# Optimization experiments

Measured on AMD Instinct MI355X. Metric: run time of the kernel, lower is better.

Reference implementation:

```python
import jax, jax.numpy as jnp
import numpy as np
from jax import lax

N_WIRES = 4
N_OPS = 30
BN_EPS = 1e-5


def _rl_ops():
    # Deterministic stand-in for tq.RandomLayer(n_ops=30): cycle rx/ry/rz/cnot.
    kinds = ['rx', 'ry', 'rz', 'cnot']
    ops, p = [], 0
    for i in range(N_OPS):
        k = kinds[i % 4]
        if k == 'cnot':
            ops.append((k, i % N_WIRES, (i + 1) % N_WIRES))
        else:
            ops.append((k, i % N_WIRES, p))
            p += 1
    return ops, p

RL_OPS, N_RL_PARAMS = _rl_ops()  # 23 rotation params, 7 cnots


def _rx(t):
    c = jnp.cos(t / 2).astype(jnp.complex64)
    s = (-1j * jnp.sin(t / 2).astype(jnp.complex64))
    return jnp.stack([jnp.stack([c, s], -1), jnp.stack([s, c], -1)], -2)


def _ry(t):
    c = jnp.cos(t / 2).astype(jnp.complex64)
    s = jnp.sin(t / 2).astype(jnp.complex64)
    return jnp.stack([jnp.stack([c, -s], -1), jnp.stack([s, c], -1)], -2)


def _rz(t):
    e = jnp.exp((-1j * t / 2).astype(jnp.complex64))
    z = jnp.zeros_like(e)
    return jnp.stack([jnp.stack([e, z], -1), jnp.stack([z, jnp.conj(e)], -1)], -2)


def _apply_1q(state, U, w):
    # state: [B,2,2,2,2]; U: [2,2] (shared) or [B,2,2] (per-sample)
    s = jnp.moveaxis(state, w + 1, -1)
    if U.ndim == 2:
        s = jnp.einsum('ij,b...j->b...i', U, s)
    else:
        s = jnp.einsum('bij,b...j->b...i', U, s)
    return jnp.moveaxis(s, -1, w + 1)


def _apply_cnot(state, c, t):
    s = jnp.moveaxis(state, (c + 1, t + 1), (-2, -1))
    s = s.at[..., 1, :].set(s[..., 1, ::-1])  # flip target where control==1
    return jnp.moveaxis(s, (-2, -1), (c + 1, t + 1))


# PauliZ expectation table: z[k, w] = +/-1 for basis state k on wire w
_ZTAB = np.array([[1.0 - 2.0 * ((k >> (N_WIRES - 1 - w)) & 1) for w in range(N_WIRES)]
                  for k in range(2 ** N_WIRES)], dtype=np.float32)  # [16,4]


def _conv(x, w, b):
    y = lax.conv_general_dilated(x, w, (1, 1), 'SAME',
                                 dimension_numbers=('NCHW', 'OIHW', 'NCHW'))
    return y + b[None, :, None, None]


def _maxpool2(x):
    return lax.reduce_window(x, -jnp.inf, lax.max, (1, 1, 2, 2), (1, 1, 2, 2), 'VALID')


def setup_inputs() -> dict:
    key = jax.random.key(0)
    ks = jax.random.split(key, 8)
    B = 8192
    return {
        'x': jax.random.normal(ks[0], (B, 1, 28, 28), jnp.float32),
        'conv1_w': jax.random.normal(ks[1], (8, 1, 3, 3), jnp.float32) * 0.1,
        'conv1_b': jnp.zeros((8,), jnp.float32),
        'conv2_w': jax.random.normal(ks[2], (16, 8, 3, 3), jnp.float32) * 0.1,
        'conv2_b': jnp.zeros((16,), jnp.float32),
        'fc1_w': jax.random.normal(ks[3], (64, 784), jnp.float32) * 0.05,
        'fc1_b': jnp.zeros((64,), jnp.float32),
        'fc2_w': jax.random.normal(ks[4], (4, 64), jnp.float32) * 0.1,
        'fc2_b': jnp.zeros((4,), jnp.float32),
        'bn_g': jnp.ones((4,), jnp.float32),
        'bn_b': jnp.zeros((4,), jnp.float32),
        'rl_params': jax.random.uniform(ks[5], (N_RL_PARAMS,), jnp.float32,
                                        -np.pi, np.pi),
    }


def reference(x, conv1_w, conv1_b, conv2_w, conv2_b, fc1_w, fc1_b,
              fc2_w, fc2_b, bn_g, bn_b, rl_params):
    B = x.shape[0]
    # CNN backbone: conv -> relu -> pool -> conv -> relu -> pool
    h = _maxpool2(jax.nn.relu(_conv(x, conv1_w, conv1_b)))          # [B,8,14,14]
    h = _maxpool2(jax.nn.relu(_conv(h, conv2_w, conv2_b)))          # [B,16,7,7]
    flat = h.reshape(B, -1)                                         # [B,784]
    h = jax.nn.relu(flat @ fc1_w.T + fc1_b)                         # [B,64]
    feat = h @ fc2_w.T + fc2_b                                      # [B,4]
    # BatchNorm1d (training mode: batch stats, biased variance)
    mean = feat.mean(0)
    var = feat.var(0)
    feat = (feat - mean) / jnp.sqrt(var + BN_EPS) * bn_g + bn_b
    # Quantum state-vector simulation on 4 wires, |0000> start
    state = jnp.zeros((B, 16), jnp.complex64).at[:, 0].set(1.0)
    state = state.reshape(B, 2, 2, 2, 2)
    # Encoder: RX(feat[:, w]) on wire w
    for w in range(N_WIRES):
        state = _apply_1q(state, _rx(feat[:, w]), w)
    # Random layer: 30 sequential gates with fixed trainable params
    gate_fns = {'rx': _rx, 'ry': _ry, 'rz': _rz}
    for kind, w, q in RL_OPS:
        if kind == 'cnot':
            state = _apply_cnot(state, w, q)
        else:
            state = _apply_1q(state, gate_fns[kind](rl_params[q]), w)
    # MeasureAll(PauliZ)
    probs = jnp.abs(state.reshape(B, 16)) ** 2                      # [B,16]
    return probs @ jnp.asarray(_ZTAB)                               # [B,4]
```

## Files before the change

kernel.cpp:

```cpp
#include <hip/hip_runtime.h>


#define B_EPS 1e-5f

__global__ void prep_kernel(const float* __restrict__ rl,
                            const float* __restrict__ f1w,
                            const float* __restrict__ c2w,
                            float* __restrict__ Uout,
                            float* __restrict__ wT2,
                            float* __restrict__ w2q,
                            float* __restrict__ stats)
{
    if (blockIdx.x == 0) {
        __shared__ float2 U[16][16];
        int t = threadIdx.x;
        int r = t >> 4, cc = t & 15;
        U[r][cc] = (r == cc) ? make_float2(1.f, 0.f) : make_float2(0.f, 0.f);
        stats[t] = 0.f;
        stats[t + 256] = 0.f;
        for (int i = t; i < 16 * 8 * 12; i += 256) {
            int ci = i / 192, rem = i - ci * 192;
            int c2 = rem / 12, qq = rem - c2 * 12;
            w2q[i] = (qq < 9) ? c2w[c2 * 72 + ci * 9 + qq] : 0.f;
        }
        __syncthreads();
        for (int op = 0; op < 30; op++) {
            int kind = op & 3;
            float2 cur = U[r][cc];
            float2 nv;
            if (kind == 3) {
                float2 part = U[r ^ 8][cc];
                nv = (r & 1) ? part : cur;
            } else {
                int m = 8 >> kind;
                float theta = rl[op - (op >> 2)];
                float ch = cosf(0.5f * theta), sh = sinf(0.5f * theta);
                float2 part = U[r ^ m][cc];
                int br = (r & m) ? 1 : 0;
                float2 gc, gp;
                if (kind == 0)      { gc = make_float2(ch, 0.f);           gp = make_float2(0.f, -sh); }
                else if (kind == 1) { gc = make_float2(ch, 0.f);           gp = make_float2(br ? sh : -sh, 0.f); }
                else                { gc = make_float2(ch, br ? sh : -sh); gp = make_float2(0.f, 0.f); }
                nv.x = gc.x*cur.x - gc.y*cur.y + gp.x*part.x - gp.y*part.y;
                nv.y = gc.x*cur.y + gc.y*cur.x + gp.x*part.y + gp.y*part.x;
            }
            __syncthreads();
            U[r][cc] = nv;
            __syncthreads();
        }
        ((float2*)Uout)[t] = U[r][cc];
    } else {
        int id = (blockIdx.x - 1) * 256 + threadIdx.x;
        if (id < 784 * 64) {
            int k = id >> 6, o = id & 63;
            wT2[(((k >> 2) * 64 + o) << 2) + (k & 3)] = f1w[o * 784 + k];
        }
    }
}

__global__ __launch_bounds__(256) void conv_kernel(
    const float* __restrict__ x,  const float* __restrict__ c1w,
    const float* __restrict__ c1b, const float* __restrict__ w2q,
    const float* __restrict__ c2b, const float* __restrict__ wT2,
    const float* __restrict__ f1b, const float* __restrict__ f2w,
    const float* __restrict__ f2bias, float* __restrict__ feat,
    float* __restrict__ stats)
{
    __shared__ union alignas(16) {
        float xin[2][30 * 32];
        float flat[2][800];
    } u;
    __shared__ union alignas(16) {
        float p1[2][8 * 292];
        struct { float part[2][4][64]; float hs[2][64]; } fc;
    } pu;

    int t = threadIdx.x;
    int w = t >> 6, lane = t & 63;

    int c1 = lane >> 3;
    float wk1[9];
    #pragma unroll
    for (int q = 0; q < 9; q++) wk1[q] = c1w[c1 * 9 + q];
    float bias1 = c1b[c1];

    {
        float4 z = make_float4(0.f, 0.f, 0.f, 0.f);
        float4* xz = (float4*)u.xin;
        for (int i = t; i < 2 * 30 * 32 / 4; i += 256) xz[i] = z;
        float4* pz = (float4*)pu.p1;
        for (int i = t; i < 2 * 8 * 292 / 4; i += 256) pz[i] = z;
    }
    __syncthreads();

    {
        const float4* xg = (const float4*)(x + (size_t)blockIdx.x * 2 * 784);
        for (int i = t; i < 392; i += 256) {
            float4 v = xg[i];
            int s = i / 196, q = (i - s * 196) * 4;
            float vv[4] = {v.x, v.y, v.z, v.w};
            #pragma unroll
            for (int j = 0; j < 4; j++) {
                int p = q + j, rr = p / 28, cc = p - rr * 28;
                u.xin[s][(rr + 1) * 32 + cc + 1] = vv[j];
            }
        }
    }
    __syncthreads();

    {
        int s = w >> 1, h = w & 1;
        int g = lane & 7;
        if (g < 7) {
            const float* xb = &u.xin[s][4 * g];
            float* pout = &pu.p1[s][c1 * 292];
            for (int ii = 0; ii < 7; ii++) {
                int i = h * 7 + ii;
                const float* r = xb + 2 * i * 32;
                float rv[4][6];
                #pragma unroll
                for (int dr = 0; dr < 4; dr++) {
                    float2 a = *(const float2*)(r + dr * 32);
                    float2 b = *(const float2*)(r + dr * 32 + 2);
                    float2 c2v = *(const float2*)(r + dr * 32 + 4);
                    rv[dr][0] = a.x;  rv[dr][1] = a.y;
                    rv[dr][2] = b.x;  rv[dr][3] = b.y;
                    rv[dr][4] = c2v.x; rv[dr][5] = c2v.y;
                }
                float o[2][4];
                #pragma unroll
                for (int dr = 0; dr < 2; dr++)
                    #pragma unroll
                    for (int j = 0; j < 4; j++) {
                        float acc = bias1;
                        #pragma unroll
                        for (int ky = 0; ky < 3; ky++)
                            #pragma unroll
                            for (int kx = 0; kx < 3; kx++)
                                acc = fmaf(wk1[ky * 3 + kx], rv[dr + ky][j + kx], acc);
                        o[dr][j] = acc;
                    }
                #pragma unroll
                for (int jj = 0; jj < 2; jj++) {
                    float m = fmaxf(fmaxf(o[0][2 * jj], o[0][2 * jj + 1]),
                                    fmaxf(o[1][2 * jj], o[1][2 * jj + 1]));
                    pout[(i + 1) * 18 + 1 + 2 * g + jj] = fmaxf(m, 0.f);
                }
            }
        }
    }
    __syncthreads();

    {
        int s = w >> 1, h = w & 1;
        int c2 = lane >> 2, g2 = lane & 3;
        int i0 = h * 4;
        float bias = c2b[c2];
        const float4* wqb = (const float4*)w2q + c2 * 3;
        float4 wa = wqb[0], wb = wqb[1], wc = wqb[2];
        float acc[4][2][4];
        #pragma unroll
        for (int ii = 0; ii < 4; ii++)
            #pragma unroll
            for (int dr = 0; dr < 2; dr++)
                #pragma unroll
                for (int j = 0; j < 4; j++) acc[ii][dr][j] = bias;

        const float* pbase = &pu.p1[s][4 * g2] + i0 * 2 * 18;
        #pragma unroll 1
        for (int ci = 0; ci < 8; ci++) {
            float wk[9] = {wa.x, wa.y, wa.z, wa.w, wb.x, wb.y, wb.z, wb.w, wc.x};
            if (ci < 7) {
                wa = wqb[(ci + 1) * 48];
                wb = wqb[(ci + 1) * 48 + 1];
                wc = wqb[(ci + 1) * 48 + 2];
            }
            const float* pc_ = pbase + ci * 292;
            #pragma unroll
            for (int ii = 0; ii < 4; ii++) {
                if (ii < 3 || h == 0) {
                    float rv[4][6];
                    #pragma unroll
                    for (int dr = 0; dr < 4; dr++) {
                        const float* rp = pc_ + (ii * 2 + dr) * 18;
                        float2 a = *(const float2*)rp;
                        float2 b = *(const float2*)(rp + 2);
                        float2 cc = *(const float2*)(rp + 4);
                        rv[dr][0] = a.x;  rv[dr][1] = a.y;
                        rv[dr][2] = b.x;  rv[dr][3] = b.y;
                        rv[dr][4] = cc.x; rv[dr][5] = cc.y;
                    }
                    #pragma unroll
                    for (int dr = 0; dr < 2; dr++)
                        #pragma unroll
                        for (int j = 0; j < 4; j++) {
                            float a2 = acc[ii][dr][j];
                            #pragma unroll
                            for (int ky = 0; ky < 3; ky++)
                                #pragma unroll
                                for (int kx = 0; kx < 3; kx++)
                                    a2 = fmaf(wk[ky * 3 + kx], rv[dr + ky][j + kx], a2);
                            acc[ii][dr][j] = a2;
                        }
                }
            }
        }
        #pragma unroll
        for (int ii = 0; ii < 4; ii++) {
            if (ii < 3 || h == 0) {
                int i = i0 + ii;
                #pragma unroll
                for (int jj = 0; jj < 2; jj++) {
                    int pc = 2 * g2 + jj;
                    if (pc < 7) {
                        float m = fmaxf(fmaxf(acc[ii][0][2 * jj], acc[ii][0][2 * jj + 1]),
                                        fmaxf(acc[ii][1][2 * jj], acc[ii][1][2 * jj + 1]));
                        u.flat[s][c2 * 49 + i * 7 + pc] = fmaxf(m, 0.f);
                    }
                }
            }
        }
    }
    __syncthreads();

    {
        const float* fl0 = u.flat[0];
        const float* fl1 = u.flat[1];
        const float4* wp4 = (const float4*)wT2 + lane;
        int g0 = w * 49;
        float a00 = 0.f, a01 = 0.f, a10 = 0.f, a11 = 0.f;
        #pragma unroll 2
        for (int g = g0; g < g0 + 48; g += 2) {
            float4 wv0 = wp4[(size_t)g * 64];
            float4 wv1 = wp4[(size_t)(g + 1) * 64];
            float4 f00 = *(const float4*)&fl0[4 * g];
            float4 f10 = *(const float4*)&fl1[4 * g];
            float4 f01 = *(const float4*)&fl0[4 * g + 4];
            float4 f11 = *(const float4*)&fl1[4 * g + 4];
            a00 = fmaf(f00.x, wv0.x, fmaf(f00.y, wv0.y, fmaf(f00.z, wv0.z, fmaf(f00.w, wv0.w, a00))));
            a10 = fmaf(f10.x, wv0.x, fmaf(f10.y, wv0.y, fmaf(f10.z, wv0.z, fmaf(f10.w, wv0.w, a10))));
            a01 = fmaf(f01.x, wv1.x, fmaf(f01.y, wv1.y, fmaf(f01.z, wv1.z, fmaf(f01.w, wv1.w, a01))));
            a11 = fmaf(f11.x, wv1.x, fmaf(f11.y, wv1.y, fmaf(f11.z, wv1.z, fmaf(f11.w, wv1.w, a11))));
        }
        {
            int g = g0 + 48;
            float4 wv = wp4[(size_t)g * 64];
            float4 f0 = *(const float4*)&fl0[4 * g];
            float4 f1 = *(const float4*)&fl1[4 * g];
            a00 = fmaf(f0.x, wv.x, fmaf(f0.y, wv.y, fmaf(f0.z, wv.z, fmaf(f0.w, wv.w, a00))));
            a10 = fmaf(f1.x, wv.x, fmaf(f1.y, wv.y, fmaf(f1.z, wv.z, fmaf(f1.w, wv.w, a10))));
        }
        pu.fc.part[0][w][lane] = a00 + a01;
        pu.fc.part[1][w][lane] = a10 + a11;
    }
    __syncthreads();

    if (t < 128) {
        int s2 = t >> 6, o = t & 63;
        float h = pu.fc.part[s2][0][o] + pu.fc.part[s2][1][o]
                + pu.fc.part[s2][2][o] + pu.fc.part[s2][3][o] + f1b[o];
        pu.fc.hs[s2][o] = fmaxf(h, 0.f);
    }
    __syncthreads();

    if (t < 8) {
        int s = t >> 2, j = t & 3;
        float a = f2bias[j];
        #pragma unroll
        for (int o = 0; o < 64; o++) a = fmaf(pu.fc.hs[s][o], f2w[j * 64 + o], a);
        feat[((size_t)blockIdx.x * 2 + s) * 4 + j] = a;
        int g = blockIdx.x & 63;
        atomicAdd(&stats[g * 8 + j], a);
        atomicAdd(&stats[g * 8 + 4 + j], a * a);
    }
}

__global__ __launch_bounds__(128) void quantum_kernel(
    const float* __restrict__ feat, const float* __restrict__ Ug,
    const float* __restrict__ stats, const float* __restrict__ bn_g,
    const float* __restrict__ bn_b, float* __restrict__ out, int B)
{
    __shared__ float2 Us[256];
    __shared__ float sm[8];
    int t = threadIdx.x;
    for (int i = t; i < 256; i += 128) Us[i] = ((const float2*)Ug)[i];
    if (t < 8) sm[t] = 0.f;
    __syncthreads();
    {
        float v = stats[t] + stats[t + 128] + stats[t + 256] + stats[t + 384];
        atomicAdd(&sm[t & 7], v);
    }
    __syncthreads();
    int q = t & 3;
    int s = blockIdx.x * 32 + (t >> 2);
    float4 fv = ((const float4*)feat)[s];
    float f[4] = {fv.x, fv.y, fv.z, fv.w};
    float cn[4], sn[4];
    float invB = 1.0f / (float)B;
    #pragma unroll
    for (int w = 0; w < 4; w++) {
        float mean = sm[w] * invB;
        float var  = sm[4 + w] * invB - mean * mean;
        float fh = (f[w] - mean) / sqrtf(var + B_EPS) * bn_g[w] + bn_b[w];
        cn[w] = cosf(0.5f * fh);
        sn[w] = sinf(0.5f * fh);
    }
    float re0[16], im0[16];
    #pragma unroll
    for (int k = 0; k < 16; k++) {
        float mag = ((k & 8) ? sn[0] : cn[0]) * ((k & 4) ? sn[1] : cn[1]) *
                    ((k & 2) ? sn[2] : cn[2]) * ((k & 1) ? sn[3] : cn[3]);
        int m = __popc(k) & 3;
        re0[k] = (m == 0) ? mag : (m == 2) ? -mag : 0.f;
        im0[k] = (m == 1) ? -mag : (m == 3) ? mag : 0.f;
    }
    float o0 = 0.f, o1 = 0.f, o2 = 0.f, o3 = 0.f;
    #pragma unroll
    for (int i = 0; i < 4; i++) {
        int r = q * 4 + i;
        float ar = 0.f, ai = 0.f;
        #pragma unroll
        for (int k = 0; k < 16; k++) {
            float2 uu = Us[r * 16 + k];
            ar += uu.x * re0[k] - uu.y * im0[k];
            ai += uu.x * im0[k] + uu.y * re0[k];
        }
        float p = ar * ar + ai * ai;
        o0 += (r & 8) ? -p : p;
        o1 += (r & 4) ? -p : p;
        o2 += (r & 2) ? -p : p;
        o3 += (r & 1) ? -p : p;
    }
    o0 += __shfl_xor(o0, 1);  o0 += __shfl_xor(o0, 2);
    o1 += __shfl_xor(o1, 1);  o1 += __shfl_xor(o1, 2);
    o2 += __shfl_xor(o2, 1);  o2 += __shfl_xor(o2, 2);
    o3 += __shfl_xor(o3, 1);  o3 += __shfl_xor(o3, 2);
    if (q == 0) {
        float4 ov = {o0, o1, o2, o3};
        ((float4*)out)[s] = ov;
    }
}

extern "C" void kernel_launch(void* const* d_in, const int* in_sizes, int n_in,
                              void* d_out, int out_size, void* d_ws, size_t ws_size,
                              hipStream_t stream)
{
    const float* x   = (const float*)d_in[0];
    const float* c1w = (const float*)d_in[1];
    const float* c1b = (const float*)d_in[2];
    const float* c2w = (const float*)d_in[3];
    const float* c2b = (const float*)d_in[4];
    const float* f1w = (const float*)d_in[5];
    const float* f1b = (const float*)d_in[6];
    const float* f2w = (const float*)d_in[7];
    const float* f2b = (const float*)d_in[8];
    const float* bng = (const float*)d_in[9];
    const float* bnb = (const float*)d_in[10];
    const float* rl  = (const float*)d_in[11];
    float* out = (float*)d_out;

    int B = in_sizes[0] / 784;

    float* wsf   = (float*)d_ws;
    float* feat  = wsf;
    float* wT2   = feat + (size_t)B * 4;
    float* U     = wT2 + 784 * 64;
    float* stats = U + 512;
    float* w2q   = stats + 512;

    prep_kernel<<<197, 256, 0, stream>>>(rl, f1w, c2w, U, wT2, w2q, stats);
    conv_kernel<<<B / 2, 256, 0, stream>>>(x, c1w, c1b, w2q, c2b, wT2,
                                           f1b, f2w, f2b, feat, stats);
    quantum_kernel<<<B / 32, 128, 0, stream>>>(feat, U, stats, bng, bnb, out, B);
}
```

Measured before the change: 202.1 us.

## Interleave two samples in shared memory and use packed FP32 FMA

The conv/FC kernel now stores its two samples interleaved as float2 pairs in shared memory and computes both at once with packed 2-wide FMA/max operations. Work is redistributed so each warp handles rows across both samples instead of splitting samples by warp. The aim is to halve the instruction count through packed math (v_pk_fma_f32) and to share weight broadcasts across samples. The change adds register pressure and alters the shared-memory padding layout.

Result: faster. 190.4 us (-5.8%).

```diff
diff --git a/kernel.cpp b/kernel.cpp
--- a/kernel.cpp
+++ b/kernel.cpp
@@ -2,6 +2,23 @@
 
 
 #define B_EPS 1e-5f
+
+typedef float f2 __attribute__((ext_vector_type(2)));
+
+__device__ __forceinline__ f2 sp(float x)          { f2 r; r.x = x; r.y = x; return r; }
+__device__ __forceinline__ f2 mk(float a, float b) { f2 r; r.x = a; r.y = b; return r; }
+#define PKFMA(a, b, c) __builtin_elementwise_fma(a, b, c)
+#define PKMAX(a, b)    __builtin_elementwise_max(a, b)
+
+__device__ __forceinline__ void row_fma(f2* acc, const float* wp, const f2* rv)
+{
+    #pragma unroll
+    for (int j = 0; j < 4; j++) {
+        acc[j] = PKFMA(sp(wp[0]), rv[j],     acc[j]);
+        acc[j] = PKFMA(sp(wp[1]), rv[j + 1], acc[j]);
+        acc[j] = PKFMA(sp(wp[2]), rv[j + 2], acc[j]);
+    }
+}
 
 __global__ void prep_kernel(const float* __restrict__ rl,
                             const float* __restrict__ f1w,
@@ -67,12 +84,12 @@
     float* __restrict__ stats)
 {
     __shared__ union alignas(16) {
-        float xin[2][30 * 32];
-        float flat[2][800];
+        f2 xin[30 * 32];
+        f2 flat[784];
     } u;
     __shared__ union alignas(16) {
-        float p1[2][8 * 292];
-        struct { float part[2][4][64]; float hs[2][64]; } fc;
+        f2 p1[8 * 290];
+        struct { f2 part[4][64]; f2 hs[64]; } fc;
     } pu;
 
     int t = threadIdx.x;
@@ -87,64 +104,54 @@
     {
         float4 z = make_float4(0.f, 0.f, 0.f, 0.f);
         float4* xz = (float4*)u.xin;
-        for (int i = t; i < 2 * 30 * 32 / 4; i += 256) xz[i] = z;
+        for (int i = t; i < 480; i += 256) xz[i] = z;
         float4* pz = (float4*)pu.p1;
-        for (int i = t; i < 2 * 8 * 292 / 4; i += 256) pz[i] = z;
-    }
-    __syncthreads();
-
-    {
-        const float4* xg = (const float4*)(x + (size_t)blockIdx.x * 2 * 784);
-        for (int i = t; i < 392; i += 256) {
-            float4 v = xg[i];
-            int s = i / 196, q = (i - s * 196) * 4;
-            float vv[4] = {v.x, v.y, v.z, v.w};
-            #pragma unroll
-            for (int j = 0; j < 4; j++) {
-                int p = q + j, rr = p / 28, cc = p - rr * 28;
-                u.xin[s][(rr + 1) * 32 + cc + 1] = vv[j];
-            }
-        }
-    }
-    __syncthreads();
-
-    {
-        int s = w >> 1, h = w & 1;
+        for (int i = t; i < 1160; i += 256) pz[i] = z;
+    }
+    __syncthreads();
+
+    {
+        const float4* xg0 = (const float4*)(x + (size_t)blockIdx.x * 2 * 784);
+        const float4* xg1 = xg0 + 196;
+        if (t < 196) {
+            float4 v0 = xg0[t];
+            float4 v1 = xg1[t];
+            int p = 4 * t, rr = p / 28, cb = p - rr * 28;
+            float4* dst = (float4*)&u.xin[(rr + 1) * 32 + cb + 2];
+            dst[0] = make_float4(v0.x, v1.x, v0.y, v1.y);
+            dst[1] = make_float4(v0.z, v1.z, v0.w, v1.w);
+        }
+    }
+    __syncthreads();
+
+    {
         int g = lane & 7;
         if (g < 7) {
-            const float* xb = &u.xin[s][4 * g];
-            float* pout = &pu.p1[s][c1 * 292];
-            for (int ii = 0; ii < 7; ii++) {
-                int i = h * 7 + ii;
-                const float* r = xb + 2 * i * 32;
-                float rv[4][6];
-                #pragma unroll
-                for (int dr = 0; dr < 4; dr++) {
-                    float2 a = *(const float2*)(r + dr * 32);
-                    float2 b = *(const float2*)(r + dr * 32 + 2);
-                    float2 c2v = *(const float2*)(r + dr * 32 + 4);
-                    rv[dr][0] = a.x;  rv[dr][1] = a.y;
-                    rv[dr][2] = b.x;  rv[dr][3] = b.y;
-                    rv[dr][4] = c2v.x; rv[dr][5] = c2v.y;
-                }
-                float o[2][4];
+            const f2* xb = &u.xin[4 * g + 1];
+            f2* pout = &pu.p1[c1 * 290 + 1];
+            #pragma unroll 1
+            for (int k = 0; k < 4; k++) {
+                int i = w + 4 * k;
+                if (i > 13) break;
+                f2 o_[2][4];
                 #pragma unroll
                 for (int dr = 0; dr < 2; dr++)
                     #pragma unroll
-                    for (int j = 0; j < 4; j++) {
-                        float acc = bias1;
-                        #pragma unroll
-                        for (int ky = 0; ky < 3; ky++)
-                            #pragma unroll
-                            for (int kx = 0; kx < 3; kx++)
-                                acc = fmaf(wk1[ky * 3 + kx], rv[dr + ky][j + kx], acc);
-                        o[dr][j] = acc;
-                    }
+                    for (int j = 0; j < 4; j++) o_[dr][j] = sp(bias1);
+                #pragma unroll
+                for (int q = 0; q < 4; q++) {
+                    f2 rv[6];
+                    const f2* rp = xb + (2 * i + q) * 32;
+                    #pragma unroll
+                    for (int m = 0; m < 6; m++) rv[m] = rp[m];
+                    if (q < 3)  row_fma(o_[0], &wk1[q * 3], rv);
+                    if (q >= 1) row_fma(o_[1], &wk1[(q - 1) * 3], rv);
+                }
                 #pragma unroll
                 for (int jj = 0; jj < 2; jj++) {
-                    float m = fmaxf(fmaxf(o[0][2 * jj], o[0][2 * jj + 1]),
-                                    fmaxf(o[1][2 * jj], o[1][2 * jj + 1]));
-                    pout[(i + 1) * 18 + 1 + 2 * g + jj] = fmaxf(m, 0.f);
+                    f2 m = PKMAX(PKMAX(o_[0][2 * jj], o_[0][2 * jj + 1]),
+                                 PKMAX(o_[1][2 * jj], o_[1][2 * jj + 1]));
+                    pout[(i + 1) * 18 + 2 * g + jj] = PKMAX(m, sp(0.f));
                 }
             }
         }
@@ -152,126 +159,104 @@
     __syncthreads();
 
     {
-        int s = w >> 1, h = w & 1;
         int c2 = lane >> 2, g2 = lane & 3;
-        int i0 = h * 4;
-        float bias = c2b[c2];
+        float bias2 = c2b[c2];
         const float4* wqb = (const float4*)w2q + c2 * 3;
-        float4 wa = wqb[0], wb = wqb[1], wc = wqb[2];
-        float acc[4][2][4];
-        #pragma unroll
-        for (int ii = 0; ii < 4; ii++)
+        #pragma unroll 1
+        for (int k = 0; k < 2; k++) {
+            int i = w + 4 * k;
+            if (i > 6) break;
+            f2 acc[2][4];
             #pragma unroll
             for (int dr = 0; dr < 2; dr++)
                 #pragma unroll
-                for (int j = 0; j < 4; j++) acc[ii][dr][j] = bias;
-
-        const float* pbase = &pu.p1[s][4 * g2] + i0 * 2 * 18;
-        #pragma unroll 1
-        for (int ci = 0; ci < 8; ci++) {
-            float wk[9] = {wa.x, wa.y, wa.z, wa.w, wb.x, wb.y, wb.z, wb.w, wc.x};
-            if (ci < 7) {
-                wa = wqb[(ci + 1) * 48];
-                wb = wqb[(ci + 1) * 48 + 1];
-                wc = wqb[(ci + 1) * 48 + 2];
+                for (int j = 0; j < 4; j++) acc[dr][j] = sp(bias2);
+            float4 wa = wqb[0], wb = wqb[1], wc = wqb[2];
+            #pragma unroll 1
+            for (int ci = 0; ci < 8; ci++) {
+                float wk[9] = {wa.x, wa.y, wa.z, wa.w, wb.x, wb.y, wb.z, wb.w, wc.x};
+                if (ci < 7) {
+                    wa = wqb[(ci + 1) * 48];
+                    wb = wqb[(ci + 1) * 48 + 1];
+                    wc = wqb[(ci + 1) * 48 + 2];
+                }
+                const f2* pc_ = &pu.p1[ci * 290 + (2 * i) * 18 + 4 * g2];
+                #pragma unroll
+                for (int q = 0; q < 4; q++) {
+                    f2 rv[6];
+                    const f2* rp = pc_ + q * 18;
+                    #pragma unroll
+                    for (int m = 0; m < 6; m++) rv[m] = rp[m];
+                    if (q < 3)  row_fma(acc[0], &wk[q * 3], rv);
+                    if (q >= 1) row_fma(acc[1], &wk[(q - 1) * 3], rv);
+                }
             }
-            const float* pc_ = pbase + ci * 292;
             #pragma unroll
-            for (int ii = 0; ii < 4; ii++) {
-                if (ii < 3 || h == 0) {
-                    float rv[4][6];
-                    #pragma unroll
-                    for (int dr = 0; dr < 4; dr++) {
-                        const float* rp = pc_ + (ii * 2 + dr) * 18;
-                        float2 a = *(const float2*)rp;
-                        float2 b = *(const float2*)(rp + 2);
-                        float2 cc = *(const float2*)(rp + 4);
-                        rv[dr][0] = a.x;  rv[dr][1] = a.y;
-                        rv[dr][2] = b.x;  rv[dr][3] = b.y;
-                        rv[dr][4] = cc.x; rv[dr][5] = cc.y;
-                    }
-                    #pragma unroll
-                    for (int dr = 0; dr < 2; dr++)
-                        #pragma unroll
-                        for (int j = 0; j < 4; j++) {
-                            float a2 = acc[ii][dr][j];
-                            #pragma unroll
-                            for (int ky = 0; ky < 3; ky++)
-                                #pragma unroll
-                                for (int kx = 0; kx < 3; kx++)
-                                    a2 = fmaf(wk[ky * 3 + kx], rv[dr + ky][j + kx], a2);
-                            acc[ii][dr][j] = a2;
-                        }
+            for (int jj = 0; jj < 2; jj++) {
+                int pc = 2 * g2 + jj;
+                if (pc < 7) {
+                    f2 m = PKMAX(PKMAX(acc[0][2 * jj], acc[0][2 * jj + 1]),
+                                 PKMAX(acc[1][2 * jj], acc[1][2 * jj + 1]));
+                    u.flat[c2 * 49 + i * 7 + pc] = PKMAX(m, sp(0.f));
                 }
             }
         }
-        #pragma unroll
-        for (int ii = 0; ii < 4; ii++) {
-            if (ii < 3 || h == 0) {
-                int i = i0 + ii;
-                #pragma unroll
-                for (int jj = 0; jj < 2; jj++) {
-                    int pc = 2 * g2 + jj;
-                    if (pc < 7) {
-                        float m = fmaxf(fmaxf(acc[ii][0][2 * jj], acc[ii][0][2 * jj + 1]),
-                                        fmaxf(acc[ii][1][2 * jj], acc[ii][1][2 * jj + 1]));
-                        u.flat[s][c2 * 49 + i * 7 + pc] = fmaxf(m, 0.f);
-                    }
-                }
-            }
-        }
-    }
-    __syncthreads();
-
-    {
-        const float* fl0 = u.flat[0];
-        const float* fl1 = u.flat[1];
+    }
+    __syncthreads();
+
+    {
+        const f2* fl = u.flat;
         const float4* wp4 = (const float4*)wT2 + lane;
         int g0 = w * 49;
-        float a00 = 0.f, a01 = 0.f, a10 = 0.f, a11 = 0.f;
+        f2 a0 = sp(0.f), a1 = sp(0.f);
         #pragma unroll 2
         for (int g = g0; g < g0 + 48; g += 2) {
             float4 wv0 = wp4[(size_t)g * 64];
             float4 wv1 = wp4[(size_t)(g + 1) * 64];
-            float4 f00 = *(const float4*)&fl0[4 * g];
-            float4 f10 = *(const float4*)&fl1[4 * g];
-            float4 f01 = *(const float4*)&fl0[4 * g + 4];
-            float4 f11 = *(const float4*)&fl1[4 * g + 4];
-            a00 = fmaf(f00.x, wv0.x, fmaf(f00.y, wv0.y, fmaf(f00.z, wv0.z, fmaf(f00.w, wv0.w, a00))));
-            a10 = fmaf(f10.x, wv0.x, fmaf(f10.y, wv0.y, fmaf(f10.z, wv0.z, fmaf(f10.w, wv0.w, a10))));
-            a01 = fmaf(f01.x, wv1.x, fmaf(f01.y, wv1.y, fmaf(f01.z, wv1.z, fmaf(f01.w, wv1.w, a01))));
-            a11 = fmaf(f11.x, wv1.x, fmaf(f11.y, wv1.y, fmaf(f11.z, wv1.z, fmaf(f11.w, wv1.w, a11))));
+            float4 fA = *(const float4*)&fl[4 * g];
+            float4 fB = *(const float4*)&fl[4 * g + 2];
+            float4 fC = *(const float4*)&fl[4 * g + 4];
+            float4 fD = *(const float4*)&fl[4 * g + 6];
+            a0 = PKFMA(sp(wv0.x), mk(fA.x, fA.y), a0);
+            a0 = PKFMA(sp(wv0.y), mk(fA.z, fA.w), a0);
+            a0 = PKFMA(sp(wv0.z), mk(fB.x, fB.y), a0);
+            a0 = PKFMA(sp(wv0.w), mk(fB.z, fB.w), a0);
+            a1 = PKFMA(sp(wv1.x), mk(fC.x, fC.y), a1);
+            a1 = PKFMA(sp(wv1.y), mk(fC.z, fC.w), a1);
+            a1 = PKFMA(sp(wv1.z), mk(fD.x, fD.y), a1);
+            a1 = PKFMA(sp(wv1.w), mk(fD.z, fD.w), a1);
         }
         {
             int g = g0 + 48;
             float4 wv = wp4[(size_t)g * 64];
-            float4 f0 = *(const float4*)&fl0[4 * g];
-            float4 f1 = *(const float4*)&fl1[4 * g];
-            a00 = fmaf(f0.x, wv.x, fmaf(f0.y, wv.y, fmaf(f0.z, wv.z, fmaf(f0.w, wv.w, a00))));
-            a10 = fmaf(f1.x, wv.x, fmaf(f1.y, wv.y, fmaf(f1.z, wv.z, fmaf(f1.w, wv.w, a10))));
-        }
-        pu.fc.part[0][w][lane] = a00 + a01;
-        pu.fc.part[1][w][lane] = a10 + a11;
-    }
-    __syncthreads();
-
-    if (t < 128) {
-        int s2 = t >> 6, o = t & 63;
-        float h = pu.fc.part[s2][0][o] + pu.fc.part[s2][1][o]
-                + pu.fc.part[s2][2][o] + pu.fc.part[s2][3][o] + f1b[o];
-        pu.fc.hs[s2][o] = fmaxf(h, 0.f);
-    }
-    __syncthreads();
-
-    if (t < 8) {
-        int s = t >> 2, j = t & 3;
-        float a = f2bias[j];
+            float4 fA = *(const float4*)&fl[4 * g];
+            float4 fB = *(const float4*)&fl[4 * g + 2];
+            a0 = PKFMA(sp(wv.x), mk(fA.x, fA.y), a0);
+            a0 = PKFMA(sp(wv.y), mk(fA.z, fA.w), a0);
+            a0 = PKFMA(sp(wv.z), mk(fB.x, fB.y), a0);
+            a0 = PKFMA(sp(wv.w), mk(fB.z, fB.w), a0);
+        }
+        pu.fc.part[w][lane] = a0 + a1;
+    }
+    __syncthreads();
+
+    if (t < 64) {
+        f2 h = pu.fc.part[0][t] + pu.fc.part[1][t]
+             + pu.fc.part[2][t] + pu.fc.part[3][t] + sp(f1b[t]);
+        pu.fc.hs[t] = PKMAX(h, sp(0.f));
+    }
+    __syncthreads();
+
+    if (t < 4) {
+        int j = t;
+        f2 a = sp(f2bias[j]);
         #pragma unroll
-        for (int o = 0; o < 64; o++) a = fmaf(pu.fc.hs[s][o], f2w[j * 64 + o], a);
-        feat[((size_t)blockIdx.x * 2 + s) * 4 + j] = a;
+        for (int o = 0; o < 64; o++) a = PKFMA(sp(f2w[j * 64 + o]), pu.fc.hs[o], a);
+        feat[((size_t)blockIdx.x * 2 + 0) * 4 + j] = a.x;
+        feat[((size_t)blockIdx.x * 2 + 1) * 4 + j] = a.y;
         int g = blockIdx.x & 63;
-        atomicAdd(&stats[g * 8 + j], a);
-        atomicAdd(&stats[g * 8 + 4 + j], a * a);
+        atomicAdd(&stats[g * 8 + j], a.x + a.y);
+        atomicAdd(&stats[g * 8 + 4 + j], a.x * a.x + a.y * a.y);
     }
 }
 
```
